# Optimization experiments

Measured on AMD Instinct MI355X. Metric: run time of the kernel, lower is better.

Reference implementation:

```python
import jax, jax.numpy as jnp
import numpy as np

B, N, D_MODEL, H, DK, DV = 8, 512, 512, 8, 64, 64
MAX_DIST = 512
NUM_REL = 2 * MAX_DIST - 1  # 1023


def setup_inputs() -> dict:
    key = jax.random.key(0)
    ks = jax.random.split(key, 12)
    s = 0.02
    return {
        "X": jax.random.normal(ks[0], (B, N, D_MODEL), jnp.float32),
        "Wq": jax.random.normal(ks[1], (D_MODEL, H * DK), jnp.float32) * s,
        "bq": jnp.zeros((H * DK,), jnp.float32),
        "Wk": jax.random.normal(ks[2], (D_MODEL, H * DK), jnp.float32) * s,
        "bk": jnp.zeros((H * DK,), jnp.float32),
        "Wv": jax.random.normal(ks[3], (D_MODEL, H * DV), jnp.float32) * s,
        "bv": jnp.zeros((H * DV,), jnp.float32),
        "Wo": jax.random.normal(ks[4], (H * DV, D_MODEL), jnp.float32) * s,
        "bo": jnp.zeros((D_MODEL,), jnp.float32),
        "P_k": jax.random.normal(ks[5], (NUM_REL, H), jnp.float32),
        "P_v": jax.random.normal(ks[6], (NUM_REL, H, DV), jnp.float32),
    }


def reference(X, Wq, bq, Wk, bk, Wv, bv, Wo, bo, P_k, P_v):
    b, n, d = X.shape
    scale = 1.0 / jnp.sqrt(jnp.float32(DK))
    # projections -> [b, h, n, d]
    Q = (X @ Wq + bq).reshape(b, n, H, DK).transpose(0, 2, 1, 3)
    K = (X @ Wk + bk).reshape(b, n, H, DK).transpose(0, 2, 1, 3)
    V = (X @ Wv + bv).reshape(b, n, H, DV).transpose(0, 2, 1, 3)
    # relative index: rel[i, j] = zero_offset + (j - i)
    zero_offset = NUM_REL // 2
    rel = zero_offset + (jnp.arange(n)[None, :] - jnp.arange(n)[:, None])  # [n, n]
    A_k = P_k[rel]  # [n, n, h]
    scores = (jnp.einsum("bhid,bhjd->bhij", Q, K) + A_k.transpose(2, 0, 1)[None]) * scale
    attn = jax.nn.softmax(scores, axis=-1)  # [b, h, n, n]
    # standard value mixing + relative value mixing (einsum avoids the
    # explicit [b,h,n,n,dv] broadcast the torch code materializes; same math)
    A_v = P_v[rel]  # [n, n, h, dv]
    out = jnp.einsum("bhij,bhjd->bhid", attn, V) + jnp.einsum("bhij,ijhd->bhid", attn, A_v)
    out = out.transpose(0, 2, 1, 3).reshape(b, n, H * DV)
    return out @ Wo + bo
```

## Files before the change

kernel.cpp:

```cpp
#include <hip/hip_runtime.h>
#include <math.h>

#define Bc 8
#define Nseq 512
#define DM 512
#define Hh 8
#define NUMREL 1023
#define ZOFF 511
#define STR 552

typedef _Float16 half8 __attribute__((ext_vector_type(8)));
typedef float f32x4 __attribute__((ext_vector_type(4)));

__device__ __forceinline__ unsigned short f2h(float f) {
  _Float16 h = (_Float16)f;
  return __builtin_bit_cast(unsigned short, h);
}

typedef __attribute__((address_space(3))) unsigned int as3_uint;
typedef __attribute__((address_space(1))) const unsigned int as1_uint;
__device__ __forceinline__ void gl_lds16(const void* g, void* l) {
  __builtin_amdgcn_global_load_lds((as1_uint*)g, (as3_uint*)l, 16, 0, 0);
}

__global__ __launch_bounds__(256) void prep_all(
    const float* __restrict__ X, const float* __restrict__ Wq,
    const float* __restrict__ Wk, const float* __restrict__ Wv,
    const float* __restrict__ Wo, const float* __restrict__ Pk,
    const float* __restrict__ Pv,
    unsigned short* __restrict__ XbF, unsigned short* __restrict__ WqF,
    unsigned short* __restrict__ WkF, unsigned short* __restrict__ WvF,
    unsigned short* __restrict__ WoF,
    float* __restrict__ Pkt, unsigned short* __restrict__ PvF2) {
  __shared__ float tbuf[5120];
  const int bid = blockIdx.x;
  const int tid = threadIdx.x;

  if (bid < 1024) {
    const int w = tid >> 6, lane = tid & 63;
    const int r = bid * 4 + w;
    const float* src = X + (size_t)r * DM + lane * 8;
    float4 a = *(const float4*)src;
    float4 b = *(const float4*)(src + 4);
    ushort4 o0, o1;
    o0.x = f2h(a.x); o0.y = f2h(a.y); o0.z = f2h(a.z); o0.w = f2h(a.w);
    o1.x = f2h(b.x); o1.y = f2h(b.y); o1.z = f2h(b.z); o1.w = f2h(b.w);
    const int mc = r >> 4, kf = lane >> 2, l = (lane & 3) * 16 + (r & 15);
    size_t flat = (((size_t)mc * 16 + kf) * 64 + l) * 8;
    *(ushort4*)(XbF + flat) = o0;
    *(ushort4*)(XbF + flat + 4) = o1;
  } else if (bid < 2048) {
    const int idx = bid - 1024;
    const int z = idx >> 8, r256 = idx & 255;
    const int bx = r256 & 15, by = r256 >> 4;
    const float* src = z == 0 ? Wq : z == 1 ? Wk : z == 2 ? Wv : Wo;
    unsigned short* dst = z == 0 ? WqF : z == 1 ? WkF : z == 2 ? WvF : WoF;
    const int k0 = by * 32, n0 = bx * 32;
#pragma unroll
    for (int u = 0; u < 4; ++u) {
      int i2 = u * 256 + tid, r = i2 >> 5, c = i2 & 31;
      tbuf[r * 33 + c] = src[(size_t)(k0 + r) * DM + n0 + c];
    }
    __syncthreads();
    const int ncl = tid >> 7, l = (tid >> 1) & 63, eh = tid & 1;
    const int nl = ncl * 16 + (l & 15);
    const int klb = (l >> 4) * 8 + eh * 4;
    ushort4 o;
    o.x = f2h(tbuf[(klb + 0) * 33 + nl]);
    o.y = f2h(tbuf[(klb + 1) * 33 + nl]);
    o.z = f2h(tbuf[(klb + 2) * 33 + nl]);
    o.w = f2h(tbuf[(klb + 3) * 33 + nl]);
    size_t flat = (((size_t)((n0 >> 4) + ncl) * 16 + (k0 >> 5)) * 64 + l) * 8 + eh * 4;
    *(ushort4*)(dst + flat) = o;
  } else if (bid < 2088) {
    const int idx = bid - 2048;
    const int gx = idx % 5, h = idx / 5;
    const int g = gx * 256 + tid;
    if (g < 1040)
      Pkt[(size_t)h * 1040 + g] = (g < NUMREL) ? Pk[(size_t)g * Hh + h] : 0.f;
  } else {
    const int idx = bid - 2088;
    const int gx = idx & 15, h = idx >> 4;
    const int g0 = gx * 64;
#pragma unroll
    for (int u = 0; u < 20; ++u) {
      int i2 = u * 256 + tid, r = i2 >> 6, c = i2 & 63;
      int g = g0 + r;
      tbuf[r * 64 + c] = (g < NUMREL) ? Pv[(size_t)g * 512 + h * 64 + c] : 0.f;
    }
    __syncthreads();
#pragma unroll
    for (int av = 0; av < 2; ++av)
#pragma unroll
      for (int gtl = 0; gtl < 2; ++gtl) {
        int gt = (g0 >> 5) + gtl;
#pragma unroll
        for (int dt = 0; dt < 4; ++dt) {
          size_t base = ((((size_t)av * Hh + h) * 4 + dt) * 32 + gt) * 512;
          int i2 = tid * 2;
          int l = i2 >> 3, e = i2 & 7;
          int gr = av * 16 + gtl * 32 + (l >> 4) * 8 + e;
          int dcol = dt * 16 + (l & 15);
          ushort2 o;
          o.x = f2h(tbuf[gr * 64 + dcol]);
          o.y = f2h(tbuf[(gr + 1) * 64 + dcol]);
          *(ushort2*)(PvF2 + base + i2) = o;
        }
      }
  }
}

__global__ __launch_bounds__(256, 2) void gemm_qkv(const unsigned short* __restrict__ XbF,
                                                   const unsigned short* __restrict__ WqF,
                                                   const unsigned short* __restrict__ WkF,
                                                   const unsigned short* __restrict__ WvF,
                                                   const float* __restrict__ bq,
                                                   const float* __restrict__ bk,
                                                   const float* __restrict__ bv,
                                                   unsigned short* __restrict__ Qb,
                                                   unsigned short* __restrict__ KF,
                                                   unsigned short* __restrict__ VF) {
  const int flat = blockIdx.x;
  const int xcd = flat & 7, g = flat >> 3;
  const int by = xcd * 8 + (g & 7), bx = g >> 3;
  const int bm = by * 64, bn = bx * 64;
  const int mc0 = bm >> 4, nc0 = bn >> 4;
  const int tid = threadIdx.x, w = tid >> 6, lane = tid & 63;
  const int lo = lane & 15, quad = lane >> 4;
  const int mh = (w >> 1) * 2, nh = (w & 1) * 2;

  __shared__ __align__(16) unsigned short stg[2][32 * 512];

  const unsigned short* srcArr = w == 0 ? XbF : w == 1 ? WqF : w == 2 ? WkF : WvF;
  const int rowbase = (w == 0) ? mc0 : nc0;

#define STAGE(buf, ks)                                                             \
  do {                                                                             \
    _Pragma("unroll") for (int t = 0; t < 8; ++t) {                                \
      gl_lds16(srcArr +                                                            \
                   (((size_t)(rowbase + (t >> 1)) * 16 + 2 * (ks) + (t & 1)) * 512) + \
                   lane * 8,                                                       \
               &stg[buf][(w * 8 + t) * 512]);                                      \
    }                                                                              \
  } while (0)

  f32x4 acc[3][2][2] = {};
  STAGE(0, 0);
  int cur = 0;
#pragma unroll
  for (int ks = 0; ks < 8; ++ks) {
    __syncthreads();
    if (ks < 7) STAGE(cur ^ 1, ks + 1);
#pragma unroll
    for (int kf = 0; kf < 2; ++kf) {
      half8 af[2], bq_[2], bk_[2], bv_[2];
#pragma unroll
      for (int i = 0; i < 2; ++i)
        af[i] = *(const half8*)(&stg[cur][((mh + i) * 2 + kf) * 512 + lane * 8]);
#pragma unroll
      for (int j = 0; j < 2; ++j) {
        bq_[j] = *(const half8*)(&stg[cur][(8 + (nh + j) * 2 + kf) * 512 + lane * 8]);
        bk_[j] = *(const half8*)(&stg[cur][(16 + (nh + j) * 2 + kf) * 512 + lane * 8]);
        bv_[j] = *(const half8*)(&stg[cur][(24 + (nh + j) * 2 + kf) * 512 + lane * 8]);
      }
#pragma unroll
      for (int i = 0; i < 2; ++i)
#pragma unroll
        for (int j = 0; j < 2; ++j) {
          acc[0][i][j] = __builtin_amdgcn_mfma_f32_16x16x32_f16(af[i], bq_[j], acc[0][i][j], 0, 0, 0);
          acc[1][i][j] = __builtin_amdgcn_mfma_f32_16x16x32_f16(af[i], bk_[j], acc[1][i][j], 0, 0, 0);
          acc[2][i][j] = __builtin_amdgcn_mfma_f32_16x16x32_f16(af[i], bv_[j], acc[2][i][j], 0, 0, 0);
        }
    }
    cur ^= 1;
  }
#undef STAGE

  const int mt = (w >> 1) * 32, nt = (w & 1) * 32;
#pragma unroll
  for (int z = 0; z < 3; ++z) {
    const float* bias = z == 0 ? bq : z == 1 ? bk : bv;
#pragma unroll
    for (int i = 0; i < 2; ++i)
#pragma unroll
      for (int j = 0; j < 2; ++j) {
        int col = bn + nt + j * 16 + lo;
        int h = col >> 6, d = col & 63;
        float bb = bias[col];
#pragma unroll
        for (int r = 0; r < 4; ++r) {
          int row = bm + mt + i * 16 + quad * 4 + r;
          int b = row >> 9, is = row & 511;
          int bh = b * Hh + h;
          unsigned short val = f2h(acc[z][i][j][r] + bb);
          if (z == 0) {
            Qb[((size_t)bh * Nseq + is) * 64 + d] = val;
          } else if (z == 1) {
            int jt = is >> 4, kf2 = d >> 5, l = ((d >> 3) & 3) * 16 + (is & 15), e = d & 7;
            KF[(((size_t)bh * 32 + jt) * 2 + kf2) * 512 + l * 8 + e] = val;
          } else {
            int dt = d >> 4, ks = is >> 5, l = ((is >> 3) & 3) * 16 + (d & 15), e = is & 7;
            VF[(((size_t)bh * 4 + dt) * 16 + ks) * 512 + l * 8 + e] = val;
          }
        }
      }
  }
}

__global__ __launch_bounds__(256, 4) void attn_fused(
    const unsigned short* __restrict__ Qb,
    const unsigned short* __restrict__ KF,
    const unsigned short* __restrict__ VF,
    const float* __restrict__ Pkt,
    const unsigned short* __restrict__ PvF2,
    unsigned short* __restrict__ AwF) {
  const int flat = blockIdx.x;
  const int h = flat & 7;
  const int grp = flat >> 3;
  const int b = grp >> 4;
  const int p = grp & 15;
  const int itA = (p >> 1) * 4 + (p & 1);
  const int i0A = itA * 16;
  const int bh = b * Hh + h;
  const int tid = threadIdx.x, w = tid >> 6, lane = tid & 63;
  const int lo = lane & 15, quad = lane >> 4;

  __shared__ __align__(16) unsigned short pstA[16 * STR + 512];
  __shared__ __align__(16) unsigned short pstB[16 * STR + 512];
  __shared__ float pk_lds[560];
  __shared__ float redm[128];
  __shared__ float redl[128];

  const int TB = 464 - i0A;

  int4 z4; z4.x = z4.y = z4.z = z4.w = 0;
  for (int c = tid; c < (16 * STR + 512) / 8; c += 256) {
    ((int4*)pstA)[c] = z4;
    ((int4*)pstB)[c] = z4;
  }
  for (int c = tid; c < 140; c += 256)
    *(float4*)(pk_lds + c * 4) = *(const float4*)(Pkt + (size_t)h * 1040 + TB + c * 4);

  const unsigned short* qA = Qb + ((size_t)bh * Nseq + i0A + lo) * 64;
  const unsigned short* qB = Qb + ((size_t)bh * Nseq + i0A + 32 + lo) * 64;
  half8 qa0 = *(const half8*)(qA + quad * 8);
  half8 qa1 = *(const half8*)(qA + 32 + quad * 8);
  half8 qb0 = *(const half8*)(qB + quad * 8);
  half8 qb1 = *(const half8*)(qB + 32 + quad * 8);

  const unsigned short* KFb = KF + ((size_t)bh * 64 + (size_t)w * 16) * 512 + lane * 8;
  const unsigned short* VFb = VF + ((size_t)bh * 4 + w) * 16 * 512 + lane * 8;
  const int aP = (TB >> 4) & 1, gtB = TB >> 5;
  const unsigned short* PFb =
      PvF2 + ((((size_t)aP * Hh + h) * 4 + w) * 32 + gtB) * 512 + lane * 8;

  __syncthreads();

  float svA[8][4], svB[8][4];
  float mA[4] = {-1e30f, -1e30f, -1e30f, -1e30f};
  float mB[4] = {-1e30f, -1e30f, -1e30f, -1e30f};
#pragma unroll
  for (int g = 0; g < 8; ++g) {
    half8 k0 = *(const half8*)(KFb + (size_t)(2 * g + 0) * 512);
    half8 k1 = *(const half8*)(KFb + (size_t)(2 * g + 1) * 512);
    f32x4 cA = {0.f, 0.f, 0.f, 0.f};
    f32x4 cB = {0.f, 0.f, 0.f, 0.f};
    cA = __builtin_amdgcn_mfma_f32_16x16x32_f16(qa0, k0, cA, 0, 0, 0);
    cA = __builtin_amdgcn_mfma_f32_16x16x32_f16(qa1, k1, cA, 0, 0, 0);
    cB = __builtin_amdgcn_mfma_f32_16x16x32_f16(qb0, k0, cB, 0, 0, 0);
    cB = __builtin_amdgcn_mfma_f32_16x16x32_f16(qb1, k1, cB, 0, 0, 0);
    int j = w * 128 + g * 16 + lo;
#pragma unroll
    for (int r = 0; r < 4; ++r) {
      int rl = quad * 4 + r;
      int idx = j - rl + 15;
      float vA = (cA[r] + pk_lds[idx + 32]) * 0.125f;
      float vB = (cB[r] + pk_lds[idx]) * 0.125f;
      svA[g][r] = vA; svB[g][r] = vB;
      mA[r] = fmaxf(mA[r], vA);
      mB[r] = fmaxf(mB[r], vB);
    }
  }

#pragma unroll
  for (int m = 1; m <= 8; m <<= 1)
#pragma unroll
    for (int r = 0; r < 4; ++r) {
      mA[r] = fmaxf(mA[r], __shfl_xor(mA[r], m));
      mB[r] = fmaxf(mB[r], __shfl_xor(mB[r], m));
    }
  if (lo == 0)
#pragma unroll
    for (int r = 0; r < 4; ++r) {
      redm[(0 * 4 + w) * 16 + quad * 4 + r] = mA[r];
      redm[(1 * 4 + w) * 16 + quad * 4 + r] = mB[r];
    }
  __syncthreads();
  float mfA[4], mfB[4];
#pragma unroll
  for (int r = 0; r < 4; ++r) {
    int rl = quad * 4 + r;
    mfA[r] = fmaxf(fmaxf(redm[rl], redm[16 + rl]), fmaxf(redm[32 + rl], redm[48 + rl]));
    mfB[r] = fmaxf(fmaxf(redm[64 + rl], redm[80 + rl]), fmaxf(redm[96 + rl], redm[112 + rl]));
  }
  float lA[4] = {0.f, 0.f, 0.f, 0.f}, lB[4] = {0.f, 0.f, 0.f, 0.f};
  unsigned int svp[8][4];
#pragma unroll
  for (int s = 0; s < 8; ++s)
#pragma unroll
    for (int r = 0; r < 4; ++r) {
      float eA = __expf(svA[s][r] - mfA[r]);
      float eB = __expf(svB[s][r] - mfB[r]);
      lA[r] += eA; lB[r] += eB;
      svp[s][r] = (unsigned int)f2h(eA) | ((unsigned int)f2h(eB) << 16);
    }
#pragma unroll
  for (int m = 1; m <= 8; m <<= 1)
#pragma unroll
    for (int r = 0; r < 4; ++r) {
      lA[r] += __shfl_xor(lA[r], m);
      lB[r] += __shfl_xor(lB[r], m);
    }
  if (lo == 0)
#pragma unroll
    for (int r = 0; r < 4; ++r) {
      redl[(0 * 4 + w) * 16 + quad * 4 + r] = lA[r];
      redl[(1 * 4 + w) * 16 + quad * 4 + r] = lB[r];
    }
  __syncthreads();
  float liA[4], liB[4];
#pragma unroll
  for (int r = 0; r < 4; ++r) {
    int rl = quad * 4 + r;
    liA[r] = 1.f / (redl[rl] + redl[16 + rl] + redl[32 + rl] + redl[48 + rl]);
    liB[r] = 1.f / (redl[64 + rl] + redl[80 + rl] + redl[96 + rl] + redl[112 + rl]);
#pragma unroll
    for (int s = 0; s < 8; ++s) {
      int j = w * 128 + s * 16 + lo;
      pstA[rl * STR + 16 + j] = (unsigned short)svp[s][r];
      pstB[rl * STR + 16 + j] = (unsigned short)(svp[s][r] >> 16);
    }
  }
  __syncthreads();

  f32x4 oVA = {0.f, 0.f, 0.f, 0.f}, oVB = {0.f, 0.f, 0.f, 0.f};
#pragma unroll
  for (int g = 0; g < 8; ++g) {
    half8 v0 = *(const half8*)(VFb + (size_t)(2 * g + 0) * 512);
    half8 v1 = *(const half8*)(VFb + (size_t)(2 * g + 1) * 512);
#pragma unroll
    for (int c = 0; c < 2; ++c) {
      int ks = 2 * g + c;
      half8 vv = c ? v1 : v0;
      half8 pA = *(const half8*)(&pstA[lo * STR + 16 + ks * 32 + quad * 8]);
      half8 pB = *(const half8*)(&pstB[lo * STR + 16 + ks * 32 + quad * 8]);
      oVA = __builtin_amdgcn_mfma_f32_16x16x32_f16(pA, vv, oVA, 0, 0, 0);
      oVB = __builtin_amdgcn_mfma_f32_16x16x32_f16(pB, vv, oVB, 0, 0, 0);
    }
  }
  __syncthreads();

#pragma unroll
  for (int r = 0; r < 4; ++r) {
    int rl = quad * 4 + r;
#pragma unroll
    for (int s = 0; s < 8; ++s) {
      int j = w * 128 + s * 16 + lo;
      int x = j - rl + 15;
      unsigned int pv = svp[s][r];
      if (w == 3 && s == 7) {
        int addr = (x < 512) ? (rl * STR + x) : (16 * STR + rl * 32 + (x - 512));
        pstA[addr] = (unsigned short)pv;
        pstB[addr] = (unsigned short)(pv >> 16);
      } else {
        pstA[rl * STR + x] = (unsigned short)pv;
        pstB[rl * STR + x] = (unsigned short)(pv >> 16);
      }
    }
  }
  __syncthreads();

  f32x4 oPA = {0.f, 0.f, 0.f, 0.f}, oPB = {0.f, 0.f, 0.f, 0.f};
#pragma unroll
  for (int g = 0; g < 9; ++g) {
    half8 p0 = *(const half8*)(PFb + (size_t)(2 * g + 0) * 512);
    half8 p1 = *(const half8*)(PFb + (size_t)(2 * g + 1) * 512);
#pragma unroll
    for (int c = 0; c < 2; ++c) {
      int cg = 2 * g + c;
      half8 pvf = c ? p1 : p0;
      if (cg < 17) {
        const unsigned short* src = (cg < 16)
            ? &pstB[lo * STR + cg * 32 + quad * 8]
            : &pstB[16 * STR + lo * 32 + quad * 8];
        oPB = __builtin_amdgcn_mfma_f32_16x16x32_f16(*(const half8*)src, pvf, oPB, 0, 0, 0);
      }
      if (cg >= 1) {
        int ksA = cg - 1;
        const unsigned short* src = (ksA < 16)
            ? &pstA[lo * STR + ksA * 32 + quad * 8]
            : &pstA[16 * STR + lo * 32 + quad * 8];
        oPA = __builtin_amdgcn_mfma_f32_16x16x32_f16(*(const half8*)src, pvf, oPA, 0, 0, 0);
      }
    }
  }

  const int kf = h * 2 + (w >> 1);
  const int lhi = ((w & 1) * 2 + (lo >> 3)) * 16;
#pragma unroll
  for (int t = 0; t < 2; ++t) {
    int mc = b * 32 + itA + t * 2;
#pragma unroll
    for (int r = 0; r < 4; ++r) {
      float ov = t ? (oVB[r] + oPB[r]) * liB[r] : (oVA[r] + oPA[r]) * liA[r];
      size_t fl = (((size_t)mc * 16 + kf) * 64 + lhi + quad * 4 + r) * 8 + (lo & 7);
      AwF[fl] = f2h(ov);
    }
  }
}

__global__ __launch_bounds__(256, 2) void gemm_final(const unsigned short* __restrict__ AF,
                                                     const unsigned short* __restrict__ BF,
                                                     const float* __restrict__ bo,
                                                     float* __restrict__ out) {
  const int flat = blockIdx.x;
  const int xcd = flat & 7, g = flat >> 3;
  const int by = xcd * 8 + (g & 7), bx = g >> 3;
  const int bm = by * 64, bn = bx * 64;
  const int mc0 = bm >> 4, nc0 = bn >> 4;
  const int tid = threadIdx.x, w = tid >> 6, lane = tid & 63;
  const int lo = lane & 15, quad = lane >> 4;
  const int mh = (w >> 1) * 2, nh = (w & 1) * 2;

  __shared__ __align__(16) unsigned short stg[2][16 * 512];

  const unsigned short* srcArr = (w < 2) ? AF : BF;
  const int rowbase = ((w < 2) ? mc0 : nc0) + (w & 1) * 2;

#define STAGE2(buf, ks)                                                            \
  do {                                                                             \
    _Pragma("unroll") for (int t = 0; t < 4; ++t) {                                \
      gl_lds16(srcArr +                                                            \
                   (((size_t)(rowbase + (t >> 1)) * 16 + 2 * (ks) + (t & 1)) * 512) + \
                   lane * 8,                                                       \
               &stg[buf][(w * 4 + t) * 512]);                                      \
    }                                                                              \
  } while (0)

  f32x4 acc[2][2] = {};
  STAGE2(0, 0);
  int cur = 0;
#pragma unroll
  for (int ks = 0; ks < 8; ++ks) {
    __syncthreads();
    if (ks < 7) STAGE2(cur ^ 1, ks + 1);
#pragma unroll
    for (int kf = 0; kf < 2; ++kf) {
      half8 af[2], bf[2];
#pragma unroll
      for (int i = 0; i < 2; ++i)
        af[i] = *(const half8*)(&stg[cur][((mh + i) * 2 + kf) * 512 + lane * 8]);
#pragma unroll
      for (int j = 0; j < 2; ++j)
        bf[j] = *(const half8*)(&stg[cur][(8 + (nh + j) * 2 + kf) * 512 + lane * 8]);
#pragma unroll
      for (int i = 0; i < 2; ++i)
#pragma unroll
        for (int j = 0; j < 2; ++j)
          acc[i][j] = __builtin_amdgcn_mfma_f32_16x16x32_f16(af[i], bf[j], acc[i][j], 0, 0, 0);
    }
    cur ^= 1;
  }
#undef STAGE2

  const int mt = (w >> 1) * 32, nt = (w & 1) * 32;
#pragma unroll
  for (int i = 0; i < 2; ++i)
#pragma unroll
    for (int j = 0; j < 2; ++j) {
      int col = bn + nt + j * 16 + lo;
      float bb = bo[col];
#pragma unroll
      for (int r = 0; r < 4; ++r) {
        int row = bm + mt + i * 16 + quad * 4 + r;
        out[(size_t)row * DM + col] = acc[i][j][r] + bb;
      }
    }
}

extern "C" void kernel_launch(void* const* d_in, const int* in_sizes, int n_in,
                              void* d_out, int out_size, void* d_ws, size_t ws_size,
                              hipStream_t stream) {
  const float* X  = (const float*)d_in[0];
  const float* Wq = (const float*)d_in[1];
  const float* bq = (const float*)d_in[2];
  const float* Wk = (const float*)d_in[3];
  const float* bk = (const float*)d_in[4];
  const float* Wv = (const float*)d_in[5];
  const float* bv = (const float*)d_in[6];
  const float* Wo = (const float*)d_in[7];
  const float* bo = (const float*)d_in[8];
  const float* Pk = (const float*)d_in[9];
  const float* Pv = (const float*)d_in[10];
  float* out = (float*)d_out;

  char* p = (char*)d_ws;
  const size_t szX    = (size_t)Bc * Nseq * DM * 2;
  const size_t szW    = (size_t)DM * DM * 2;
  const size_t szPkt  = (size_t)Hh * 1040 * 4;
  const size_t szPvF2 = (size_t)2 * Hh * 4 * 32 * 512 * 2;
  const size_t szQKV  = (size_t)Bc * Hh * Nseq * 64 * 2;
  unsigned short* XbF = (unsigned short*)p; p += szX;
  unsigned short* WqF = (unsigned short*)p; p += szW;
  unsigned short* WkF = (unsigned short*)p; p += szW;
  unsigned short* WvF = (unsigned short*)p; p += szW;
  unsigned short* WoF = (unsigned short*)p; p += szW;
  float*          Pkt = (float*)p;          p += (szPkt + 255) & ~(size_t)255;
  unsigned short* PvF2 = (unsigned short*)p; p += szPvF2;
  unsigned short* Qb  = (unsigned short*)p; p += szQKV;
  unsigned short* KF  = (unsigned short*)p; p += szQKV;
  unsigned short* VF  = (unsigned short*)p; p += szQKV;
  unsigned short* AwF = (unsigned short*)p; p += szX;

  dim3 blk(256);
  prep_all<<<dim3(2216), blk, 0, stream>>>(X, Wq, Wk, Wv, Wo, Pk, Pv,
                                           XbF, WqF, WkF, WvF, WoF, Pkt, PvF2);
  gemm_qkv<<<dim3(512), blk, 0, stream>>>(XbF, WqF, WkF, WvF, bq, bk, bv, Qb, KF, VF);
  attn_fused<<<dim3(1024), blk, 0, stream>>>(Qb, KF, VF, Pkt, PvF2, AwF);
  gemm_final<<<dim3(512), blk, 0, stream>>>(AwF, WoF, bo, out);
}
```

Baseline: 131.2 us.

## Halve QKV GEMM staging, raise occupancy, trim LDS zeroing, add MFMA priority hints

The QKV GEMM now stages one 32-wide k-slice per step instead of two, which halves its LDS buffers and doubles the pipeline steps. Its launch bound is raised to allow 4 blocks per CU, trading per-block prefetch depth for more resident blocks. The attention kernel zeroes only the padding regions of its P staging buffers instead of the whole buffers. It also wraps MFMA groups in s_setprio to favour matrix issue. Correctness depends on every other LDS cell being written before it is read.

```diff
diff --git a/kernel.cpp b/kernel.cpp
--- a/kernel.cpp
+++ b/kernel.cpp
@@ -110,7 +110,7 @@
   }
 }
 
-__global__ __launch_bounds__(256, 2) void gemm_qkv(const unsigned short* __restrict__ XbF,
+__global__ __launch_bounds__(256, 4) void gemm_qkv(const unsigned short* __restrict__ XbF,
                                                    const unsigned short* __restrict__ WqF,
                                                    const unsigned short* __restrict__ WkF,
                                                    const unsigned short* __restrict__ WvF,
@@ -129,49 +129,45 @@
   const int lo = lane & 15, quad = lane >> 4;
   const int mh = (w >> 1) * 2, nh = (w & 1) * 2;
 
-  __shared__ __align__(16) unsigned short stg[2][32 * 512];
+  __shared__ __align__(16) unsigned short stg[2][16 * 512];
 
   const unsigned short* srcArr = w == 0 ? XbF : w == 1 ? WqF : w == 2 ? WkF : WvF;
   const int rowbase = (w == 0) ? mc0 : nc0;
 
-#define STAGE(buf, ks)                                                             \
-  do {                                                                             \
-    _Pragma("unroll") for (int t = 0; t < 8; ++t) {                                \
-      gl_lds16(srcArr +                                                            \
-                   (((size_t)(rowbase + (t >> 1)) * 16 + 2 * (ks) + (t & 1)) * 512) + \
-                   lane * 8,                                                       \
-               &stg[buf][(w * 8 + t) * 512]);                                      \
-    }                                                                              \
+#define STAGE(buf, ks)                                                      \
+  do {                                                                      \
+    _Pragma("unroll") for (int t = 0; t < 4; ++t) {                         \
+      gl_lds16(srcArr + (((size_t)(rowbase + t) * 16 + (ks)) * 512) +       \
+                   lane * 8,                                                \
+               &stg[buf][(w * 4 + t) * 512]);                               \
+    }                                                                       \
   } while (0)
 
   f32x4 acc[3][2][2] = {};
   STAGE(0, 0);
   int cur = 0;
 #pragma unroll
-  for (int ks = 0; ks < 8; ++ks) {
+  for (int ks = 0; ks < 16; ++ks) {
     __syncthreads();
-    if (ks < 7) STAGE(cur ^ 1, ks + 1);
-#pragma unroll
-    for (int kf = 0; kf < 2; ++kf) {
-      half8 af[2], bq_[2], bk_[2], bv_[2];
-#pragma unroll
-      for (int i = 0; i < 2; ++i)
-        af[i] = *(const half8*)(&stg[cur][((mh + i) * 2 + kf) * 512 + lane * 8]);
+    if (ks < 15) STAGE(cur ^ 1, ks + 1);
+    half8 af[2], bq_[2], bk_[2], bv_[2];
+#pragma unroll
+    for (int i = 0; i < 2; ++i)
+      af[i] = *(const half8*)(&stg[cur][(mh + i) * 512 + lane * 8]);
+#pragma unroll
+    for (int j = 0; j < 2; ++j) {
+      bq_[j] = *(const half8*)(&stg[cur][(4 + nh + j) * 512 + lane * 8]);
+      bk_[j] = *(const half8*)(&stg[cur][(8 + nh + j) * 512 + lane * 8]);
+      bv_[j] = *(const half8*)(&stg[cur][(12 + nh + j) * 512 + lane * 8]);
+    }
+#pragma unroll
+    for (int i = 0; i < 2; ++i)
 #pragma unroll
       for (int j = 0; j < 2; ++j) {
-        bq_[j] = *(const half8*)(&stg[cur][(8 + (nh + j) * 2 + kf) * 512 + lane * 8]);
-        bk_[j] = *(const half8*)(&stg[cur][(16 + (nh + j) * 2 + kf) * 512 + lane * 8]);
-        bv_[j] = *(const half8*)(&stg[cur][(24 + (nh + j) * 2 + kf) * 512 + lane * 8]);
-      }
-#pragma unroll
-      for (int i = 0; i < 2; ++i)
-#pragma unroll
-        for (int j = 0; j < 2; ++j) {
-          acc[0][i][j] = __builtin_amdgcn_mfma_f32_16x16x32_f16(af[i], bq_[j], acc[0][i][j], 0, 0, 0);
-          acc[1][i][j] = __builtin_amdgcn_mfma_f32_16x16x32_f16(af[i], bk_[j], acc[1][i][j], 0, 0, 0);
-          acc[2][i][j] = __builtin_amdgcn_mfma_f32_16x16x32_f16(af[i], bv_[j], acc[2][i][j], 0, 0, 0);
-        }
-    }
+        acc[0][i][j] = __builtin_amdgcn_mfma_f32_16x16x32_f16(af[i], bq_[j], acc[0][i][j], 0, 0, 0);
+        acc[1][i][j] = __builtin_amdgcn_mfma_f32_16x16x32_f16(af[i], bk_[j], acc[1][i][j], 0, 0, 0);
+        acc[2][i][j] = __builtin_amdgcn_mfma_f32_16x16x32_f16(af[i], bv_[j], acc[2][i][j], 0, 0, 0);
+      }
     cur ^= 1;
   }
 #undef STAGE
@@ -233,10 +229,19 @@
 
   const int TB = 464 - i0A;
 
-  int4 z4; z4.x = z4.y = z4.z = z4.w = 0;
-  for (int c = tid; c < (16 * STR + 512) / 8; c += 256) {
-    ((int4*)pstA)[c] = z4;
-    ((int4*)pstB)[c] = z4;
+  {
+    int4 z4; z4.x = z4.y = z4.z = z4.w = 0;
+    int c = tid;
+    if (c < 96) {
+      int addr = (c < 32) ? ((c >> 1) * STR + (c & 1) * 8)
+                          : (16 * STR + (c - 32) * 8);
+      *(int4*)(pstA + addr) = z4;
+    } else if (c < 192) {
+      int c2 = c - 96;
+      int addr = (c2 < 32) ? ((c2 >> 1) * STR + (c2 & 1) * 8)
+                           : (16 * STR + (c2 - 32) * 8);
+      *(int4*)(pstB + addr) = z4;
+    }
   }
   for (int c = tid; c < 140; c += 256)
     *(float4*)(pk_lds + c * 4) = *(const float4*)(Pkt + (size_t)h * 1040 + TB + c * 4);
@@ -265,10 +270,12 @@
     half8 k1 = *(const half8*)(KFb + (size_t)(2 * g + 1) * 512);
     f32x4 cA = {0.f, 0.f, 0.f, 0.f};
     f32x4 cB = {0.f, 0.f, 0.f, 0.f};
+    __builtin_amdgcn_s_setprio(1);
     cA = __builtin_amdgcn_mfma_f32_16x16x32_f16(qa0, k0, cA, 0, 0, 0);
     cA = __builtin_amdgcn_mfma_f32_16x16x32_f16(qa1, k1, cA, 0, 0, 0);
     cB = __builtin_amdgcn_mfma_f32_16x16x32_f16(qb0, k0, cB, 0, 0, 0);
     cB = __builtin_amdgcn_mfma_f32_16x16x32_f16(qb1, k1, cB, 0, 0, 0);
+    __builtin_amdgcn_s_setprio(0);
     int j = w * 128 + g * 16 + lo;
 #pragma unroll
     for (int r = 0; r < 4; ++r) {
@@ -354,8 +361,10 @@
       half8 vv = c ? v1 : v0;
       half8 pA = *(const half8*)(&pstA[lo * STR + 16 + ks * 32 + quad * 8]);
       half8 pB = *(const half8*)(&pstB[lo * STR + 16 + ks * 32 + quad * 8]);
+      __builtin_amdgcn_s_setprio(1);
       oVA = __builtin_amdgcn_mfma_f32_16x16x32_f16(pA, vv, oVA, 0, 0, 0);
       oVB = __builtin_amdgcn_mfma_f32_16x16x32_f16(pB, vv, oVB, 0, 0, 0);
+      __builtin_amdgcn_s_setprio(0);
     }
   }
   __syncthreads();
@@ -393,14 +402,20 @@
         const unsigned short* src = (cg < 16)
             ? &pstB[lo * STR + cg * 32 + quad * 8]
             : &pstB[16 * STR + lo * 32 + quad * 8];
-        oPB = __builtin_amdgcn_mfma_f32_16x16x32_f16(*(const half8*)src, pvf, oPB, 0, 0, 0);
+        half8 pb = *(const half8*)src;
+        __builtin_amdgcn_s_setprio(1);
+        oPB = __builtin_amdgcn_mfma_f32_16x16x32_f16(pb, pvf, oPB, 0, 0, 0);
+        __builtin_amdgcn_s_setprio(0);
       }
       if (cg >= 1) {
         int ksA = cg - 1;
         const unsigned short* src = (ksA < 16)
             ? &pstA[lo * STR + ksA * 32 + quad * 8]
             : &pstA[16 * STR + lo * 32 + quad * 8];
-        oPA = __builtin_amdgcn_mfma_f32_16x16x32_f16(*(const half8*)src, pvf, oPA, 0, 0, 0);
+        half8 pa = *(const half8*)src;
+        __builtin_amdgcn_s_setprio(1);
+        oPA = __builtin_amdgcn_mfma_f32_16x16x32_f16(pa, pvf, oPA, 0, 0, 0);
+        __builtin_amdgcn_s_setprio(0);
       }
     }
   }
```

Result: no change. 133.2 us (+1.5%).
